# Performance work log

Hardware: AMD Instinct MI355X
Metric: run time of the kernel (lower is better)

Reference implementation:

```python
import jax, jax.numpy as jnp
import numpy as np


def setup_inputs() -> dict:
    key = jax.random.key(0)
    k1, k2 = jax.random.split(key)
    B, L, D = 8, 4096, 1024
    hidden = jax.random.normal(k1, (B, L, D), dtype=jnp.float32)
    w1 = jax.random.normal(k2, (D // 2 + 1,), dtype=jnp.float32)
    return {"hidden": hidden, "w1": w1}


def reference(hidden, w1):
    # hidden: [B, L, D]; w1: [D//2+1]
    B, L, D = hidden.shape
    flat = hidden.reshape(-1, D)                 # [B*L, D]
    Xf1 = jnp.fft.rfft(flat, axis=1)             # [B*L, D//2+1] complex
    gate = jax.nn.softmax(w1, axis=0)[None, :]   # [1, D//2+1]
    t1 = jnp.fft.irfft(Xf1 * gate, n=D, axis=1)  # [B*L, D]
    return t1.reshape(B, L, D).astype(hidden.dtype)
```

## Files before the change

### kernel.cpp

```cpp
#include <hip/hip_runtime.h>


__device__ __forceinline__ int sw(int a) {
    return a ^ (int)((((unsigned)a >> 6) * 9u) & 31u);
}

template <bool INV>
__device__ __forceinline__ void bfly8(float* xr, float* xi)
{
    const float r2 = 0.70710678118654752f;
    float t0r = xr[0] + xr[4], t0i = xi[0] + xi[4];
    float t1r = xr[0] - xr[4], t1i = xi[0] - xi[4];
    float t2r = xr[2] + xr[6], t2i = xi[2] + xi[6];
    float t3r = xr[2] - xr[6], t3i = xi[2] - xi[6];
    float e0r = t0r + t2r, e0i = t0i + t2i;
    float e2r = t0r - t2r, e2i = t0i - t2i;
    float e1r, e1i, e3r, e3i;
    if (!INV) { e1r = t1r + t3i; e1i = t1i - t3r; e3r = t1r - t3i; e3i = t1i + t3r; }
    else      { e1r = t1r - t3i; e1i = t1i + t3r; e3r = t1r + t3i; e3i = t1i - t3r; }
    float s0r = xr[1] + xr[5], s0i = xi[1] + xi[5];
    float s1r = xr[1] - xr[5], s1i = xi[1] - xi[5];
    float s2r = xr[3] + xr[7], s2i = xi[3] + xi[7];
    float s3r = xr[3] - xr[7], s3i = xi[3] - xi[7];
    float o0r = s0r + s2r, o0i = s0i + s2i;
    float o2r = s0r - s2r, o2i = s0i - s2i;
    float o1r, o1i, o3r, o3i;
    if (!INV) { o1r = s1r + s3i; o1i = s1i - s3r; o3r = s1r - s3i; o3i = s1i + s3r; }
    else      { o1r = s1r - s3i; o1i = s1i + s3r; o3r = s1r + s3i; o3i = s1i - s3r; }
    float p1r, p1i, p2r, p2i, p3r, p3i;
    if (!INV) {
        p1r = (o1r + o1i) * r2;  p1i = (o1i - o1r) * r2;
        p2r = o2i;               p2i = -o2r;
        p3r = (o3i - o3r) * r2;  p3i = -(o3r + o3i) * r2;
    } else {
        p1r = (o1r - o1i) * r2;  p1i = (o1i + o1r) * r2;
        p2r = -o2i;              p2i = o2r;
        p3r = -(o3r + o3i) * r2; p3i = (o3r - o3i) * r2;
    }
    xr[0] = e0r + o0r; xi[0] = e0i + o0i;
    xr[4] = e0r - o0r; xi[4] = e0i - o0i;
    xr[1] = e1r + p1r; xi[1] = e1i + p1i;
    xr[5] = e1r - p1r; xi[5] = e1i - p1i;
    xr[2] = e2r + p2r; xi[2] = e2i + p2i;
    xr[6] = e2r - p2r; xi[6] = e2i - p2i;
    xr[3] = e3r + p3r; xi[3] = e3i + p3i;
    xr[7] = e3r - p3r; xi[7] = e3i - p3i;
}

template <bool INV>
__device__ __forceinline__ void tw_apply(float* xr, float* xi,
                                         const float* c, const float* s)
{
#pragma unroll
    for (int k = 1; k < 8; ++k) {
        float r, i;
        if (!INV) { r = xr[k] * c[k] + xi[k] * s[k]; i = xi[k] * c[k] - xr[k] * s[k]; }
        else      { r = xr[k] * c[k] - xi[k] * s[k]; i = xi[k] * c[k] + xr[k] * s[k]; }
        xr[k] = r; xi[k] = i;
    }
}

template <int S>
__device__ __forceinline__ void store_stage(int t, const float* xr, const float* xi,
                                            float* dr, float* di)
{
    int base = (t & (S - 1)) + ((t & ~(S - 1)) << 3);
#pragma unroll
    for (int k = 0; k < 8; ++k) {
        int idx = sw(base + k * S);
        dr[idx] = xr[k]; di[idx] = xi[k];
    }
}

__device__ __forceinline__ void load_stage(int t, float* xr, float* xi,
                                           const float* dr, const float* di)
{
#pragma unroll
    for (int k = 0; k < 8; ++k) {
        int idx = sw(t + 64 * k);
        xr[k] = dr[idx]; xi[k] = di[idx];
    }
}

__global__ __launch_bounds__(256)
void fv_kernel(const float2* __restrict__ x,
               const float2* __restrict__ pq,
               const float2* __restrict__ tw1,
               const float2* __restrict__ tw8,
               float2* __restrict__ out)
{
    __shared__ float Ar[4][512], Ai[4][512], Br[4][512], Bi[4][512];
    const int tid = threadIdx.x;
    const int r = tid >> 6;
    const int t = tid & 63;
    float* ar = Ar[r]; float* ai = Ai[r];
    float* br = Br[r]; float* bi = Bi[r];
    const size_t rowbase = ((size_t)blockIdx.x * 4 + r) * 512;

    float c1[8], s1[8], c8[8], s8[8];
#pragma unroll
    for (int k = 1; k < 8; ++k) {
        float2 w = tw1[(k - 1) * 64 + t];        c1[k] = w.x; s1[k] = w.y;
        float2 v = tw8[(k - 1) * 8 + (t >> 3)];  c8[k] = v.x; s8[k] = v.y;
    }

    float zr[8], zi[8];

#pragma unroll
    for (int k = 0; k < 8; ++k) {
        float2 v = x[rowbase + t + 64 * k];
        zr[k] = v.x; zi[k] = v.y;
    }
    bfly8<false>(zr, zi);
    tw_apply<false>(zr, zi, c1, s1);
    store_stage<1>(t, zr, zi, ar, ai);

    load_stage(t, zr, zi, ar, ai);
    bfly8<false>(zr, zi);
    tw_apply<false>(zr, zi, c8, s8);
    store_stage<8>(t, zr, zi, br, bi);

    load_stage(t, zr, zi, br, bi);
    bfly8<false>(zr, zi);
    store_stage<64>(t, zr, zi, ar, ai);

#pragma unroll
    for (int k = 0; k < 8; ++k) {
        int idx = t + 64 * k;
        int mir = (512 - idx) & 511;
        float ur = ar[sw(idx)], ui = ai[sw(idx)];
        float vr = ar[sw(mir)], vi = ai[sw(mir)];
        float2 g = pq[idx];
        zr[k] = g.x * ur + g.y * vi;
        zi[k] = g.x * ui + g.y * vr;
    }
    bfly8<true>(zr, zi);
    tw_apply<true>(zr, zi, c1, s1);
    store_stage<1>(t, zr, zi, br, bi);

    load_stage(t, zr, zi, br, bi);
    bfly8<true>(zr, zi);
    tw_apply<true>(zr, zi, c8, s8);
    store_stage<8>(t, zr, zi, ar, ai);

    load_stage(t, zr, zi, ar, ai);
    bfly8<true>(zr, zi);
#pragma unroll
    for (int k = 0; k < 8; ++k) {
        out[rowbase + t + 64 * k] = make_float2(zr[k], zi[k]);
    }
}

__global__ void gate_kernel(const float* __restrict__ w1,
                            float2* __restrict__ pq,
                            float2* __restrict__ tw1,
                            float2* __restrict__ tw8)
{
    __shared__ float red[1024];
    __shared__ float ex[513];
    const int t = threadIdx.x;

    float v = (t < 513) ? w1[t] : -1e30f;
    red[t] = v;
    __syncthreads();
    for (int off = 512; off > 0; off >>= 1) {
        if (t < off) red[t] = fmaxf(red[t], red[t + off]);
        __syncthreads();
    }
    float M = red[0];
    __syncthreads();

    float e = (t < 513) ? expf(w1[t] - M) : 0.0f;
    if (t < 513) ex[t] = e;
    red[t] = e;
    __syncthreads();
    for (int off = 512; off > 0; off >>= 1) {
        if (t < off) red[t] += red[t + off];
        __syncthreads();
    }
    float inv = 1.0f / red[0];
    __syncthreads();

    if (t < 512) {
        float ga = ex[t] * inv;
        float gb = ex[512 - t] * inv;
        float gp = ga + gb, gm = ga - gb;
        float th = (float)t * 3.06796157577128245e-03f;
        th = (float)t * 6.13592315154256492e-03f;
        float sn, cs;
        __sincosf(th, &sn, &cs);
        float P = 0.5f * (gp - gm * sn) * (1.0f / 512.0f);
        float q = 0.5f * (gm * cs) * (1.0f / 512.0f);
        pq[t] = make_float2(P, q);
    }
    if (t < 448) {
        int k = (t >> 6) + 1;
        int j = t & 63;
        float th = (float)(j * k) * 1.22718463151036952e-02f;
        float sn, cs;
        sincosf(th, &sn, &cs);
        tw1[t] = make_float2(cs, sn);
    }
    if (t < 56) {
        int k = (t >> 3) + 1;
        int p = t & 7;
        float th = (float)(p * k) * 9.81747704246810387e-02f;
        float sn, cs;
        sincosf(th, &sn, &cs);
        tw8[t] = make_float2(cs, sn);
    }
}

extern "C" void kernel_launch(void* const* d_in, const int* in_sizes, int n_in,
                              void* d_out, int out_size, void* d_ws, size_t ws_size,
                              hipStream_t stream)
{
    (void)n_in; (void)out_size; (void)ws_size;
    const float2* hidden = (const float2*)d_in[0];
    const float*  w1     = (const float*)d_in[1];
    float2* out = (float2*)d_out;

    float2* pq  = (float2*)d_ws;
    float2* tw1 = pq + 512;
    float2* tw8 = tw1 + 448;

    gate_kernel<<<1, 1024, 0, stream>>>(w1, pq, tw1, tw8);

    const int rows   = in_sizes[0] / 1024;
    const int blocks = rows / 4;
    fv_kernel<<<blocks, 256, 0, stream>>>(hidden, pq, tw1, tw8, out);
}
```

Baseline: 236.1 us.

## Replace XOR-swizzled shared transposes with padded layout and shuffle-based mirror gather

Swaps the XOR-swizzled double-buffered shared arrays for a single padded buffer per row, with simpler linear index patterns for each transpose stage. The mirrored-bin gather that paired each spectrum element with its conjugate partner now uses wavefront shuffles from registers instead of a shared store and reload. The goal is to cut shared-memory traffic, index arithmetic and LDS footprint in this memory-bound kernel. Reusing one buffer across stages relies on implicit wavefront-level ordering, since each row is handled by exactly one 64-lane wave.

```diff
diff --git a/kernel.cpp b/kernel.cpp
--- a/kernel.cpp
+++ b/kernel.cpp
@@ -1,14 +1,11 @@
 #include <hip/hip_runtime.h>
 
 
-__device__ __forceinline__ int sw(int a) {
-    return a ^ (int)((((unsigned)a >> 6) * 9u) & 31u);
-}
+#define R2F 0.70710678118654752f
 
 template <bool INV>
 __device__ __forceinline__ void bfly8(float* xr, float* xi)
 {
-    const float r2 = 0.70710678118654752f;
     float t0r = xr[0] + xr[4], t0i = xi[0] + xi[4];
     float t1r = xr[0] - xr[4], t1i = xi[0] - xi[4];
     float t2r = xr[2] + xr[6], t2i = xi[2] + xi[6];
@@ -29,13 +26,13 @@
     else      { o1r = s1r - s3i; o1i = s1i + s3r; o3r = s1r + s3i; o3i = s1i - s3r; }
     float p1r, p1i, p2r, p2i, p3r, p3i;
     if (!INV) {
-        p1r = (o1r + o1i) * r2;  p1i = (o1i - o1r) * r2;
-        p2r = o2i;               p2i = -o2r;
-        p3r = (o3i - o3r) * r2;  p3i = -(o3r + o3i) * r2;
+        p1r = (o1r + o1i) * R2F;  p1i = (o1i - o1r) * R2F;
+        p2r = o2i;                p2i = -o2r;
+        p3r = (o3i - o3r) * R2F;  p3i = -(o3r + o3i) * R2F;
     } else {
-        p1r = (o1r - o1i) * r2;  p1i = (o1i + o1r) * r2;
-        p2r = -o2i;              p2i = o2r;
-        p3r = -(o3r + o3i) * r2; p3i = (o3r - o3i) * r2;
+        p1r = (o1r - o1i) * R2F;  p1i = (o1i + o1r) * R2F;
+        p2r = -o2i;               p2i = o2r;
+        p3r = -(o3r + o3i) * R2F; p3i = (o3r - o3i) * R2F;
     }
     xr[0] = e0r + o0r; xi[0] = e0i + o0i;
     xr[4] = e0r - o0r; xi[4] = e0i - o0i;
@@ -60,28 +57,6 @@
     }
 }
 
-template <int S>
-__device__ __forceinline__ void store_stage(int t, const float* xr, const float* xi,
-                                            float* dr, float* di)
-{
-    int base = (t & (S - 1)) + ((t & ~(S - 1)) << 3);
-#pragma unroll
-    for (int k = 0; k < 8; ++k) {
-        int idx = sw(base + k * S);
-        dr[idx] = xr[k]; di[idx] = xi[k];
-    }
-}
-
-__device__ __forceinline__ void load_stage(int t, float* xr, float* xi,
-                                           const float* dr, const float* di)
-{
-#pragma unroll
-    for (int k = 0; k < 8; ++k) {
-        int idx = sw(t + 64 * k);
-        xr[k] = dr[idx]; xi[k] = di[idx];
-    }
-}
-
 __global__ __launch_bounds__(256)
 void fv_kernel(const float2* __restrict__ x,
                const float2* __restrict__ pq,
@@ -89,12 +64,11 @@
                const float2* __restrict__ tw8,
                float2* __restrict__ out)
 {
-    __shared__ float Ar[4][512], Ai[4][512], Br[4][512], Bi[4][512];
+    __shared__ float sre[4][544], sim[4][544];
     const int tid = threadIdx.x;
     const int r = tid >> 6;
     const int t = tid & 63;
-    float* ar = Ar[r]; float* ai = Ai[r];
-    float* br = Br[r]; float* bi = Bi[r];
+    float* re = sre[r]; float* im = sim[r];
     const size_t rowbase = ((size_t)blockIdx.x * 4 + r) * 512;
 
     float c1[8], s1[8], c8[8], s8[8];
@@ -104,6 +78,10 @@
         float2 v = tw8[(k - 1) * 8 + (t >> 3)];  c8[k] = v.x; s8[k] = v.y;
     }
 
+    const int p0 = (t << 3) + (t >> 1);
+    const int lt = t + (t >> 4);
+    const int sb = (t & 7) + 68 * (t >> 3);
+
     float zr[8], zi[8];
 
 #pragma unroll
@@ -113,37 +91,60 @@
     }
     bfly8<false>(zr, zi);
     tw_apply<false>(zr, zi, c1, s1);
-    store_stage<1>(t, zr, zi, ar, ai);
-
-    load_stage(t, zr, zi, ar, ai);
+#pragma unroll
+    for (int k = 0; k < 8; ++k) { re[p0 + k] = zr[k]; im[p0 + k] = zi[k]; }
+#pragma unroll
+    for (int k = 0; k < 8; ++k) { zr[k] = re[lt + 68 * k]; zi[k] = im[lt + 68 * k]; }
     bfly8<false>(zr, zi);
     tw_apply<false>(zr, zi, c8, s8);
-    store_stage<8>(t, zr, zi, br, bi);
-
-    load_stage(t, zr, zi, br, bi);
+#pragma unroll
+    for (int k = 0; k < 8; ++k) {
+        int a = sb + 8 * k + (k >> 1);
+        re[a] = zr[k]; im[a] = zi[k];
+    }
+#pragma unroll
+    for (int k = 0; k < 8; ++k) { zr[k] = re[lt + 68 * k]; zi[k] = im[lt + 68 * k]; }
     bfly8<false>(zr, zi);
-    store_stage<64>(t, zr, zi, ar, ai);
-
-#pragma unroll
-    for (int k = 0; k < 8; ++k) {
-        int idx = t + 64 * k;
-        int mir = (512 - idx) & 511;
-        float ur = ar[sw(idx)], ui = ai[sw(idx)];
-        float vr = ar[sw(mir)], vi = ai[sw(mir)];
-        float2 g = pq[idx];
-        zr[k] = g.x * ur + g.y * vi;
-        zi[k] = g.x * ui + g.y * vr;
-    }
+
+    {
+        const int src = (64 - t) & 63;
+        float vr[8], vi[8];
+#pragma unroll
+        for (int k = 0; k < 8; ++k) {
+            vr[k] = __shfl(zr[7 - k], src, 64);
+            vi[k] = __shfl(zi[7 - k], src, 64);
+        }
+        if (t == 0) {
+#pragma unroll
+            for (int k = 0; k < 8; ++k) {
+                int kk = (8 - k) & 7;
+                vr[k] = zr[kk]; vi[k] = zi[kk];
+            }
+        }
+#pragma unroll
+        for (int k = 0; k < 8; ++k) {
+            float2 g = pq[t + 64 * k];
+            float nr = g.x * zr[k] + g.y * vi[k];
+            float ni = g.x * zi[k] + g.y * vr[k];
+            zr[k] = nr; zi[k] = ni;
+        }
+    }
+
     bfly8<true>(zr, zi);
     tw_apply<true>(zr, zi, c1, s1);
-    store_stage<1>(t, zr, zi, br, bi);
-
-    load_stage(t, zr, zi, br, bi);
+#pragma unroll
+    for (int k = 0; k < 8; ++k) { re[p0 + k] = zr[k]; im[p0 + k] = zi[k]; }
+#pragma unroll
+    for (int k = 0; k < 8; ++k) { zr[k] = re[lt + 68 * k]; zi[k] = im[lt + 68 * k]; }
     bfly8<true>(zr, zi);
     tw_apply<true>(zr, zi, c8, s8);
-    store_stage<8>(t, zr, zi, ar, ai);
-
-    load_stage(t, zr, zi, ar, ai);
+#pragma unroll
+    for (int k = 0; k < 8; ++k) {
+        int a = sb + 8 * k + (k >> 1);
+        re[a] = zr[k]; im[a] = zi[k];
+    }
+#pragma unroll
+    for (int k = 0; k < 8; ++k) { zr[k] = re[lt + 68 * k]; zi[k] = im[lt + 68 * k]; }
     bfly8<true>(zr, zi);
 #pragma unroll
     for (int k = 0; k < 8; ++k) {
@@ -185,8 +186,7 @@
         float ga = ex[t] * inv;
         float gb = ex[512 - t] * inv;
         float gp = ga + gb, gm = ga - gb;
-        float th = (float)t * 3.06796157577128245e-03f;
-        th = (float)t * 6.13592315154256492e-03f;
+        float th = (float)t * 6.13592315154256492e-03f;
         float sn, cs;
         __sincosf(th, &sn, &cs);
         float P = 0.5f * (gp - gm * sn) * (1.0f / 512.0f);
```

Measured after the change: 234.7 us. No clear change (-0.6%).
